# Kernel optimization log

Hardware: AMD Instinct MI355X
Metric: run time of the kernel (lower is better)

The kernel has to match this reference:

```python
import jax, jax.numpy as jnp
import numpy as np

TOPK = 10
NUM_CLASSES = 80
ALPHA = 0.5
BETA = 6.0
EPS = 1e-9


def setup_inputs() -> dict:
    key = jax.random.key(0)
    ks = jax.random.split(key, 7)
    bs, A, n, C = 16, 8400, 64, NUM_CLASSES
    pd_scores = jax.random.uniform(ks[0], (bs, A, C), jnp.float32)
    # valid xyxy boxes inside a 640x640 image
    pxy = jax.random.uniform(ks[1], (bs, A, 2), jnp.float32) * 576.0
    pwh = jax.random.uniform(ks[2], (bs, A, 2), jnp.float32) * 64.0 + 8.0
    pd_bboxes = jnp.concatenate([pxy, pxy + pwh], axis=-1)
    gxy = jax.random.uniform(ks[3], (bs, n, 2), jnp.float32) * 576.0
    gwh = jax.random.uniform(ks[4], (bs, n, 2), jnp.float32) * 64.0 + 8.0
    gt_bboxes = jnp.concatenate([gxy, gxy + gwh], axis=-1)
    anc_points = jax.random.uniform(ks[5], (A, 2), jnp.float32) * 640.0
    gt_labels = jax.random.randint(ks[6], (bs, n, 1), 0, C, dtype=jnp.int32)
    return {"pd_scores": pd_scores, "pd_bboxes": pd_bboxes,
            "anc_points": anc_points, "gt_labels": gt_labels,
            "gt_bboxes": gt_bboxes}


def _iou(gt_bboxes, pd_bboxes, eps=EPS):
    # gt_bboxes: (bs, n, 4), pd_bboxes: (bs, A, 4) -> (bs, n, A)
    b1 = gt_bboxes[:, :, None, :]
    b2 = pd_bboxes[:, None, :, :]
    lt = jnp.maximum(b1[..., :2], b2[..., :2])
    rb = jnp.minimum(b1[..., 2:], b2[..., 2:])
    overlap = jnp.clip(rb - lt, 0).prod(-1)
    area1 = jnp.clip(b1[..., 2:] - b1[..., :2], 0).prod(-1)
    area2 = jnp.clip(b2[..., 2:] - b2[..., :2], 0).prod(-1)
    return overlap / (area1 + area2 - overlap + eps)


def _assign(pd_scores, pd_bboxes, anc_points, gt_labels, gt_bboxes):
    bs, A, C = pd_scores.shape
    n = gt_bboxes.shape[1]
    dt = pd_scores.dtype
    labels = gt_labels[..., 0]                       # (bs, n)
    # ---- box metrics: gather class score per gt (bs, n, A) ----
    bi = jnp.arange(bs)[:, None]                     # (bs, 1)
    bbox_scores = pd_scores[bi, :, labels]           # (bs, n, A)
    overlaps = _iou(gt_bboxes, pd_bboxes)            # (bs, n, A)
    align_metric = bbox_scores ** ALPHA * overlaps ** BETA
    # ---- anchor-center-in-gt mask ----
    lt = gt_bboxes[..., None, :2]                    # (bs, n, 1, 2)
    rb = gt_bboxes[..., None, 2:]
    anc = anc_points[None, None]                     # (1, 1, A, 2)
    deltas_min = jnp.minimum((anc - lt).min(-1), (rb - anc).min(-1))
    mask_in_gts = (deltas_min > EPS).astype(dt)      # (bs, n, A)
    # ---- top-k candidates per gt (scatter-add instead of huge one-hot) ----
    metrics = align_metric * mask_in_gts
    topk_vals, topk_idxs = jax.lax.top_k(metrics, TOPK)
    valid = topk_vals.max(-1, keepdims=True) > EPS
    topk_idxs = jnp.where(valid, topk_idxs, 0)
    bi3 = jnp.arange(bs)[:, None, None]
    ni3 = jnp.arange(n)[None, :, None]
    cnt = jnp.zeros((bs, n, A), dt).at[bi3, ni3, topk_idxs].add(1.0)
    is_in_topk = jnp.where(cnt > 1, jnp.zeros((), dt), cnt)
    mask_pos = is_in_topk * mask_in_gts
    # ---- resolve anchors assigned to multiple gts via highest IoU ----
    fg_mask = mask_pos.sum(-2)                       # (bs, A)
    mask_multi = fg_mask[:, None, :] > 1             # (bs, 1->n, A)
    is_max = jax.nn.one_hot(overlaps.argmax(1), n, axis=1, dtype=dt)  # (bs, n, A)
    mask_pos = jnp.where(mask_multi, is_max, mask_pos)
    fg_mask = mask_pos.sum(-2)
    target_gt_idx = mask_pos.argmax(-2)              # (bs, A)
    # ---- gather targets ----
    flat_idx = target_gt_idx + jnp.arange(bs)[:, None] * n
    target_labels = jnp.maximum(labels.reshape(-1)[flat_idx], 0)
    target_bboxes = gt_bboxes.reshape(-1, 4)[flat_idx]
    target_scores = jax.nn.one_hot(target_labels, C, dtype=dt)
    target_scores = jnp.where(fg_mask[..., None] > 0, target_scores,
                              jnp.zeros((), dt))
    # ---- normalize scores by task-aligned metric ----
    align_metric = align_metric * mask_pos
    pos_align = align_metric.max(-1, keepdims=True)
    pos_over = (overlaps * mask_pos).max(-1, keepdims=True)
    norm = (align_metric * pos_over / (pos_align + EPS)).max(-2)[..., None]
    target_scores = target_scores * norm
    return target_labels, target_bboxes, target_scores, fg_mask > 0


def reference(pd_scores, pd_bboxes, anc_points, gt_labels, gt_bboxes):
    return _assign(pd_scores, pd_bboxes, anc_points, gt_labels, gt_bboxes)
```

## Files before the change

### kernel.cpp

```cpp
#include <hip/hip_runtime.h>

#define TOPK 10
#define EPSF 1e-9f
#define CHUNKS 8

typedef unsigned long long u64;
typedef unsigned int u32;

__global__ __launch_bounds__(256) void k_init(uint4* __restrict__ p, int n16) {
    int i = blockIdx.x * 256 + threadIdx.x;
    if (i < n16) p[i] = make_uint4(0, 0, 0, 0);
}

__global__ __launch_bounds__(256) void k_chunk(
    const float* __restrict__ pd_scores, const float* __restrict__ pd_bboxes,
    const float* __restrict__ anc, const int* __restrict__ gt_labels,
    const float* __restrict__ gt_bboxes,
    float* __restrict__ overlaps, u64* __restrict__ part,
    int A, int n, int C)
{
    const int gw   = blockIdx.x * 4 + (threadIdx.x >> 6);
    const int lane = threadIdx.x & 63;
    const int row  = gw >> 3;
    const int ch   = gw & (CHUNKS - 1);
    const int b    = row / n;
    const int CS   = (A + CHUNKS - 1) / CHUNKS;
    const int a0   = ch * CS;
    const int a1   = min(A, a0 + CS);

    const float4 g = *(const float4*)(gt_bboxes + (size_t)row * 4);
    const int    c = gt_labels[row];
    const float* ps = pd_scores + (size_t)b * A * C + c;
    const float4* pb = (const float4*)(pd_bboxes + (size_t)b * A * 4);
    const float2* an2 = (const float2*)anc;
    const size_t rowbase = (size_t)row * A;
    const float ga = fmaxf(g.z - g.x, 0.f) * fmaxf(g.w - g.y, 0.f);

    u64 tk[TOPK];
    #pragma unroll
    for (int k = 0; k < TOPK; ++k) tk[k] = 0;

    for (int a = a0 + lane; a < a1; a += 64) {
        float4 p = pb[a];
        float ow = fmaxf(fminf(g.z, p.z) - fmaxf(g.x, p.x), 0.f) *
                   fmaxf(fminf(g.w, p.w) - fmaxf(g.y, p.y), 0.f);
        float pa = fmaxf(p.z - p.x, 0.f) * fmaxf(p.w - p.y, 0.f);
        float iou = ow / (ga + pa - ow + EPSF);
        overlaps[rowbase + a] = iou;

        float2 ap = an2[a];
        float dmin = fminf(fminf(ap.x - g.x, ap.y - g.y),
                           fminf(g.z - ap.x, g.w - ap.y));
        float met = 0.f;
        if (dmin > EPSF) met = sqrtf(ps[(size_t)a * C]) * powf(iou, 6.0f);

        u64 key = ((u64)__float_as_uint(met) << 32) | (u32)(0x7fffffff - a);
        if (key > tk[TOPK-1]) {
            tk[TOPK-1] = key;
            #pragma unroll
            for (int k = TOPK-1; k > 0; --k)
                if (tk[k] > tk[k-1]) { u64 t = tk[k]; tk[k] = tk[k-1]; tk[k-1] = t; }
        }
    }

    u64 mine = 0;
    #pragma unroll
    for (int r = 0; r < TOPK; ++r) {
        u64 m = tk[0];
        #pragma unroll
        for (int s = 1; s < 64; s <<= 1) {
            u64 o = __shfl_xor(m, s, 64);
            m = (o > m) ? o : m;
        }
        if (lane == r) mine = m;
        if (tk[0] == m) {
            #pragma unroll
            for (int k = 0; k < TOPK - 1; ++k) tk[k] = tk[k + 1];
            tk[TOPK-1] = 0;
        }
    }
    if (lane < TOPK)
        part[((size_t)row * CHUNKS + ch) * TOPK + lane] = mine;
}

__global__ __launch_bounds__(64) void k_merge(
    const float* __restrict__ anc, const float* __restrict__ gt_bboxes,
    const u64* __restrict__ part, u64* __restrict__ mask64,
    int A, int n, int R)
{
    int row = blockIdx.x * 64 + threadIdx.x;
    if (row >= R) return;
    int b = row / n;
    int j = row - b * n;
    const u64* l = part + (size_t)row * CHUNKS * TOPK;
    const float4 g = *(const float4*)(gt_bboxes + (size_t)row * 4);
    const float2* an2 = (const float2*)anc;

    int p0 = 0, p1 = 0, p2 = 0, p3 = 0, p4 = 0, p5 = 0, p6 = 0, p7 = 0;
    for (int k = 0; k < TOPK; ++k) {
        u64 v0 = (p0 < TOPK) ? l[0*TOPK + p0] : 0;
        u64 v1 = (p1 < TOPK) ? l[1*TOPK + p1] : 0;
        u64 v2 = (p2 < TOPK) ? l[2*TOPK + p2] : 0;
        u64 v3 = (p3 < TOPK) ? l[3*TOPK + p3] : 0;
        u64 v4 = (p4 < TOPK) ? l[4*TOPK + p4] : 0;
        u64 v5 = (p5 < TOPK) ? l[5*TOPK + p5] : 0;
        u64 v6 = (p6 < TOPK) ? l[6*TOPK + p6] : 0;
        u64 v7 = (p7 < TOPK) ? l[7*TOPK + p7] : 0;
        u64 bv = v0; int best = 0;
        if (v1 > bv) { bv = v1; best = 1; }
        if (v2 > bv) { bv = v2; best = 2; }
        if (v3 > bv) { bv = v3; best = 3; }
        if (v4 > bv) { bv = v4; best = 4; }
        if (v5 > bv) { bv = v5; best = 5; }
        if (v6 > bv) { bv = v6; best = 6; }
        if (v7 > bv) { bv = v7; best = 7; }
        p0 += (best == 0); p1 += (best == 1); p2 += (best == 2); p3 += (best == 3);
        p4 += (best == 4); p5 += (best == 5); p6 += (best == 6); p7 += (best == 7);

        if (k == 0) {
            float m0 = __uint_as_float((u32)(bv >> 32));
            if (!(m0 > EPSF)) break;
        }
        int a = 0x7fffffff - (int)(u32)(bv & 0xffffffffu);
        float2 ap = an2[a];
        float dmin = fminf(fminf(ap.x - g.x, ap.y - g.y),
                           fminf(g.z - ap.x, g.w - ap.y));
        if (dmin > EPSF)
            atomicOr(&mask64[(size_t)b * A + a], 1ull << j);
    }
}

__global__ __launch_bounds__(256) void k_col(
    const float* __restrict__ pd_scores,
    const int* __restrict__ gt_labels, const float* __restrict__ gt_bboxes,
    const float* __restrict__ overlaps, u64* __restrict__ mask64,
    float* __restrict__ out_labels, float* __restrict__ out_bboxes,
    float* __restrict__ out_fg,
    float* __restrict__ pos_align, float* __restrict__ pos_over,
    int A, int n, int C)
{
    __shared__ float4 sg[64];
    __shared__ int    sl[64];
    const int b = blockIdx.y;
    const int a = blockIdx.x * 256 + threadIdx.x;
    if (threadIdx.x < n) {
        sg[threadIdx.x] = ((const float4*)gt_bboxes)[b * n + threadIdx.x];
        sl[threadIdx.x] = gt_labels[b * n + threadIdx.x];
    }
    __syncthreads();
    if (a >= A) return;

    const size_t midx = (size_t)b * A + a;
    u64 m = mask64[midx];
    int pc = __popcll(m);
    int jt = 0;
    if (pc > 1) {
        const float* col = overlaps + (size_t)b * n * A + a;
        float bv = col[0]; int bj = 0;
        for (int jj = 1; jj < n; ++jj) {
            float v = col[(size_t)jj * A];
            if (v > bv) { bv = v; bj = jj; }
        }
        jt = bj; mask64[midx] = 1ull << bj; pc = 1;
    } else if (pc == 1) {
        jt = __ffsll(m) - 1;
    }

    int lab = sl[jt];
    out_labels[midx] = (float)(lab < 0 ? 0 : lab);
    ((float4*)out_bboxes)[midx] = sg[jt];
    out_fg[midx] = pc ? 1.f : 0.f;

    if (pc) {
        int rowj = b * n + jt;
        float iou = overlaps[(size_t)rowj * A + a];
        float s = pd_scores[((size_t)b * A + a) * C + lab];
        float al = sqrtf(s) * powf(iou, 6.0f);
        atomicMax((int*)&pos_align[rowj], __float_as_int(al));
        atomicMax((int*)&pos_over[rowj],  __float_as_int(iou));
    }
}

__global__ __launch_bounds__(256) void k_norm(
    const float* __restrict__ pd_scores, const int* __restrict__ gt_labels,
    const float* __restrict__ overlaps, const u64* __restrict__ mask64,
    const float* __restrict__ pos_align, const float* __restrict__ pos_over,
    float* __restrict__ normv, int A, int n, int C, int total)
{
    int idx = blockIdx.x * 256 + threadIdx.x;
    if (idx >= total) return;
    int b = idx / A;
    int a = idx - b * A;
    u64 m = mask64[idx];
    float nm = 0.f;
    if (m) {
        int jj = __ffsll(m) - 1;
        int rowj = b * n + jj;
        float iou = overlaps[(size_t)rowj * A + a];
        float s = pd_scores[(size_t)idx * C + gt_labels[rowj]];
        float al = sqrtf(s) * powf(iou, 6.0f);
        nm = al * pos_over[rowj] / (pos_align[rowj] + EPSF);
    }
    normv[idx] = nm;
}

__global__ __launch_bounds__(256) void k_scores(
    const float* __restrict__ out_labels, const float* __restrict__ out_fg,
    const float* __restrict__ normv, float4* __restrict__ out_scores,
    int C4, int quads)
{
    int idx = blockIdx.x * 256 + threadIdx.x;
    if (idx >= quads) return;
    int ba = idx / C4;
    int q  = idx - ba * C4;
    float4 v = make_float4(0.f, 0.f, 0.f, 0.f);
    if (out_fg[ba] > 0.f) {
        int r = (int)out_labels[ba] - q * 4;
        float nv = normv[ba];
        v.x = (r == 0) ? nv : 0.f;
        v.y = (r == 1) ? nv : 0.f;
        v.z = (r == 2) ? nv : 0.f;
        v.w = (r == 3) ? nv : 0.f;
    }
    out_scores[idx] = v;
}

extern "C" void kernel_launch(void* const* d_in, const int* in_sizes, int n_in,
                              void* d_out, int out_size, void* d_ws, size_t ws_size,
                              hipStream_t stream)
{
    const float* pd_scores = (const float*)d_in[0];
    const float* pd_bboxes = (const float*)d_in[1];
    const float* anc       = (const float*)d_in[2];
    const int*   gt_labels = (const int*)d_in[3];
    const float* gt_bboxes = (const float*)d_in[4];

    const int C  = 80;
    const int A  = in_sizes[2] / 2;
    const int bs = in_sizes[0] / (A * C);
    const int n  = in_sizes[3] / bs;
    const int R  = bs * n;
    const int BA = bs * A;

    size_t off = 0;
    u64*   mask64    = (u64*)((char*)d_ws + off);   off += (size_t)BA * 8;
    float* pos_align = (float*)((char*)d_ws + off); off += (size_t)R * 4;
    float* pos_over  = (float*)((char*)d_ws + off); off += (size_t)R * 4;
    size_t zero_bytes = off;
    float* overlaps  = (float*)((char*)d_ws + off); off += (size_t)R * A * 4;
    float* normv     = (float*)((char*)d_ws + off); off += (size_t)BA * 4;
    u64*   part      = (u64*)((char*)d_ws + off);   off += (size_t)R * CHUNKS * TOPK * 8;

    float* out_labels = (float*)d_out;
    float* out_bboxes = out_labels + (size_t)BA;
    float* out_scores = out_bboxes + (size_t)BA * 4;
    float* out_fg     = out_scores + (size_t)BA * C;

    int n16 = (int)(zero_bytes / 16);
    k_init<<<(n16 + 255) / 256, 256, 0, stream>>>((uint4*)d_ws, n16);

    k_chunk<<<R * CHUNKS / 4, 256, 0, stream>>>(
        pd_scores, pd_bboxes, anc, gt_labels, gt_bboxes, overlaps, part, A, n, C);

    k_merge<<<(R + 63) / 64, 64, 0, stream>>>(
        anc, gt_bboxes, part, mask64, A, n, R);

    k_col<<<dim3((A + 255) / 256, bs), 256, 0, stream>>>(
        pd_scores, gt_labels, gt_bboxes, overlaps, mask64,
        out_labels, out_bboxes, out_fg, pos_align, pos_over, A, n, C);

    k_norm<<<(BA + 255) / 256, 256, 0, stream>>>(
        pd_scores, gt_labels, overlaps, mask64, pos_align, pos_over,
        normv, A, n, C, BA);

    int quads = BA * (C / 4);
    k_scores<<<(quads + 255) / 256, 256, 0, stream>>>(
        out_labels, out_fg, normv, (float4*)out_scores, C / 4, quads);
}
```

Measured before the change: 169.0 us.

## Drop materialized overlaps buffer and recompute IoU on demand

The full (bs, n, A) overlaps array is no longer written. IoU is recomputed from the gt and pred boxes wherever it is needed: in the column argmax, the alignment atomics and the normalization. The chunk kernel now skips IoU and the score gather for anchors outside the gt box and keeps only positive metrics. A wave-parallel merge adds a fallback scan that fills zero-metric top-k slots by index order. This removes roughly 34 MB of writes and strided column reads, in exchange for n IoU evaluations per multi-assigned anchor and a more complex tie-handling path.

```diff
diff --git a/kernel.cpp b/kernel.cpp
--- a/kernel.cpp
+++ b/kernel.cpp
@@ -7,6 +7,27 @@
 typedef unsigned long long u64;
 typedef unsigned int u32;
 
+__device__ __forceinline__ float gt_area(const float4 g) {
+    return fmaxf(g.z - g.x, 0.f) * fmaxf(g.w - g.y, 0.f);
+}
+__device__ __forceinline__ float iou_pair(const float4 g, const float4 p, float ga) {
+    float ow = fmaxf(fminf(g.z, p.z) - fmaxf(g.x, p.x), 0.f) *
+               fmaxf(fminf(g.w, p.w) - fmaxf(g.y, p.y), 0.f);
+    float pa = fmaxf(p.z - p.x, 0.f) * fmaxf(p.w - p.y, 0.f);
+    return ow / (ga + pa - ow + EPSF);
+}
+__device__ __forceinline__ float dmin_f(const float4 g, const float2 ap) {
+    return fminf(fminf(ap.x - g.x, ap.y - g.y), fminf(g.z - ap.x, g.w - ap.y));
+}
+__device__ __forceinline__ u64 wave_max_u64(u64 v) {
+    #pragma unroll
+    for (int s = 1; s < 64; s <<= 1) {
+        u64 o = __shfl_xor(v, s, 64);
+        v = (o > v) ? o : v;
+    }
+    return v;
+}
+
 __global__ __launch_bounds__(256) void k_init(uint4* __restrict__ p, int n16) {
     int i = blockIdx.x * 256 + threadIdx.x;
     if (i < n16) p[i] = make_uint4(0, 0, 0, 0);
@@ -15,8 +36,7 @@
 __global__ __launch_bounds__(256) void k_chunk(
     const float* __restrict__ pd_scores, const float* __restrict__ pd_bboxes,
     const float* __restrict__ anc, const int* __restrict__ gt_labels,
-    const float* __restrict__ gt_bboxes,
-    float* __restrict__ overlaps, u64* __restrict__ part,
+    const float* __restrict__ gt_bboxes, u64* __restrict__ part,
     int A, int n, int C)
 {
     const int gw   = blockIdx.x * 4 + (threadIdx.x >> 6);
@@ -33,45 +53,35 @@
     const float* ps = pd_scores + (size_t)b * A * C + c;
     const float4* pb = (const float4*)(pd_bboxes + (size_t)b * A * 4);
     const float2* an2 = (const float2*)anc;
-    const size_t rowbase = (size_t)row * A;
-    const float ga = fmaxf(g.z - g.x, 0.f) * fmaxf(g.w - g.y, 0.f);
+    const float ga = gt_area(g);
 
     u64 tk[TOPK];
     #pragma unroll
     for (int k = 0; k < TOPK; ++k) tk[k] = 0;
 
     for (int a = a0 + lane; a < a1; a += 64) {
-        float4 p = pb[a];
-        float ow = fmaxf(fminf(g.z, p.z) - fmaxf(g.x, p.x), 0.f) *
-                   fmaxf(fminf(g.w, p.w) - fmaxf(g.y, p.y), 0.f);
-        float pa = fmaxf(p.z - p.x, 0.f) * fmaxf(p.w - p.y, 0.f);
-        float iou = ow / (ga + pa - ow + EPSF);
-        overlaps[rowbase + a] = iou;
-
         float2 ap = an2[a];
-        float dmin = fminf(fminf(ap.x - g.x, ap.y - g.y),
-                           fminf(g.z - ap.x, g.w - ap.y));
-        float met = 0.f;
-        if (dmin > EPSF) met = sqrtf(ps[(size_t)a * C]) * powf(iou, 6.0f);
-
-        u64 key = ((u64)__float_as_uint(met) << 32) | (u32)(0x7fffffff - a);
-        if (key > tk[TOPK-1]) {
-            tk[TOPK-1] = key;
-            #pragma unroll
-            for (int k = TOPK-1; k > 0; --k)
-                if (tk[k] > tk[k-1]) { u64 t = tk[k]; tk[k] = tk[k-1]; tk[k-1] = t; }
+        float dmin = dmin_f(g, ap);
+        if (dmin > EPSF) {
+            float iou = iou_pair(g, pb[a], ga);
+            float met = sqrtf(ps[(size_t)a * C]) * powf(iou, 6.0f);
+            if (met > 0.f) {
+                u64 key = ((u64)__float_as_uint(met) << 32) | (u32)(0x7fffffff - a);
+                if (key > tk[TOPK-1]) {
+                    tk[TOPK-1] = key;
+                    #pragma unroll
+                    for (int k = TOPK-1; k > 0; --k)
+                        if (tk[k] > tk[k-1]) { u64 t = tk[k]; tk[k] = tk[k-1]; tk[k-1] = t; }
+                }
+            }
         }
     }
 
     u64 mine = 0;
     #pragma unroll
     for (int r = 0; r < TOPK; ++r) {
-        u64 m = tk[0];
-        #pragma unroll
-        for (int s = 1; s < 64; s <<= 1) {
-            u64 o = __shfl_xor(m, s, 64);
-            m = (o > m) ? o : m;
-        }
+        u64 m = wave_max_u64(tk[0]);
+        if (m == 0) break;
         if (lane == r) mine = m;
         if (tk[0] == m) {
             #pragma unroll
@@ -83,57 +93,84 @@
         part[((size_t)row * CHUNKS + ch) * TOPK + lane] = mine;
 }
 
-__global__ __launch_bounds__(64) void k_merge(
-    const float* __restrict__ anc, const float* __restrict__ gt_bboxes,
+__global__ __launch_bounds__(256) void k_merge(
+    const float* __restrict__ pd_scores, const float* __restrict__ pd_bboxes,
+    const float* __restrict__ anc, const int* __restrict__ gt_labels,
+    const float* __restrict__ gt_bboxes,
     const u64* __restrict__ part, u64* __restrict__ mask64,
-    int A, int n, int R)
-{
-    int row = blockIdx.x * 64 + threadIdx.x;
-    if (row >= R) return;
-    int b = row / n;
-    int j = row - b * n;
-    const u64* l = part + (size_t)row * CHUNKS * TOPK;
+    int A, int n, int C)
+{
+    const int row  = blockIdx.x * 4 + (threadIdx.x >> 6);
+    const int lane = threadIdx.x & 63;
+    const int b    = row / n;
+    const int j    = row - b * n;
+
+    const u64* l = part + (size_t)row * (CHUNKS * TOPK);
+    u64 e0 = l[lane];
+    u64 e1 = (lane < CHUNKS * TOPK - 64) ? l[64 + lane] : 0;
+
     const float4 g = *(const float4*)(gt_bboxes + (size_t)row * 4);
+    const int    c = gt_labels[row];
+    const float* ps = pd_scores + (size_t)b * A * C + c;
+    const float4* pb = (const float4*)(pd_bboxes + (size_t)b * A * 4);
     const float2* an2 = (const float2*)anc;
-
-    int p0 = 0, p1 = 0, p2 = 0, p3 = 0, p4 = 0, p5 = 0, p6 = 0, p7 = 0;
-    for (int k = 0; k < TOPK; ++k) {
-        u64 v0 = (p0 < TOPK) ? l[0*TOPK + p0] : 0;
-        u64 v1 = (p1 < TOPK) ? l[1*TOPK + p1] : 0;
-        u64 v2 = (p2 < TOPK) ? l[2*TOPK + p2] : 0;
-        u64 v3 = (p3 < TOPK) ? l[3*TOPK + p3] : 0;
-        u64 v4 = (p4 < TOPK) ? l[4*TOPK + p4] : 0;
-        u64 v5 = (p5 < TOPK) ? l[5*TOPK + p5] : 0;
-        u64 v6 = (p6 < TOPK) ? l[6*TOPK + p6] : 0;
-        u64 v7 = (p7 < TOPK) ? l[7*TOPK + p7] : 0;
-        u64 bv = v0; int best = 0;
-        if (v1 > bv) { bv = v1; best = 1; }
-        if (v2 > bv) { bv = v2; best = 2; }
-        if (v3 > bv) { bv = v3; best = 3; }
-        if (v4 > bv) { bv = v4; best = 4; }
-        if (v5 > bv) { bv = v5; best = 5; }
-        if (v6 > bv) { bv = v6; best = 6; }
-        if (v7 > bv) { bv = v7; best = 7; }
-        p0 += (best == 0); p1 += (best == 1); p2 += (best == 2); p3 += (best == 3);
-        p4 += (best == 4); p5 += (best == 5); p6 += (best == 6); p7 += (best == 7);
-
-        if (k == 0) {
-            float m0 = __uint_as_float((u32)(bv >> 32));
-            if (!(m0 > EPSF)) break;
-        }
-        int a = 0x7fffffff - (int)(u32)(bv & 0xffffffffu);
-        float2 ap = an2[a];
-        float dmin = fminf(fminf(ap.x - g.x, ap.y - g.y),
-                           fminf(g.z - ap.x, g.w - ap.y));
-        if (dmin > EPSF)
-            atomicOr(&mask64[(size_t)b * A + a], 1ull << j);
+    const float ga = gt_area(g);
+    u64* mrow = mask64 + (size_t)b * A;
+
+    int npos = 0;
+    bool invalid = false;
+    u64 mine = 0;
+    for (int r = 0; r < TOPK; ++r) {
+        u64 me = (e0 > e1) ? e0 : e1;
+        u64 m = wave_max_u64(me);
+        if (r == 0) {
+            float m0 = __uint_as_float((u32)(m >> 32));
+            if (!(m0 > EPSF)) { invalid = true; break; }
+        }
+        if (m == 0) break;
+        if (lane == r) mine = m;
+        if (e0 == m) e0 = 0; else if (e1 == m) e1 = 0;
+        ++npos;
+    }
+
+    if (lane < npos) {
+        int a = 0x7fffffff - (int)(u32)(mine & 0xffffffffu);
+        if (dmin_f(g, an2[a]) > EPSF)
+            atomicOr(&mrow[a], 1ull << j);
+    }
+
+    if (!invalid) {
+        int need = TOPK - npos;
+        int base = 0;
+        while (need > 0 && base < A) {
+            int a = base + lane;
+            float met = 1.f;
+            float dmin = -1.f;
+            if (a < A) {
+                float2 ap = an2[a];
+                dmin = dmin_f(g, ap);
+                met = 0.f;
+                if (dmin > EPSF) {
+                    float iou = iou_pair(g, pb[a], ga);
+                    met = sqrtf(ps[(size_t)a * C]) * powf(iou, 6.0f);
+                }
+            }
+            u64 zm = __ballot(met == 0.f);
+            int cnt = __popcll(zm);
+            int take = (need < cnt) ? need : cnt;
+            int rank = __popcll(zm & ((1ull << lane) - 1ull));
+            if (met == 0.f && rank < take && dmin > EPSF)
+                atomicOr(&mrow[a], 1ull << j);
+            need -= take;
+            base += 64;
+        }
     }
 }
 
 __global__ __launch_bounds__(256) void k_col(
-    const float* __restrict__ pd_scores,
+    const float* __restrict__ pd_scores, const float* __restrict__ pd_bboxes,
     const int* __restrict__ gt_labels, const float* __restrict__ gt_bboxes,
-    const float* __restrict__ overlaps, u64* __restrict__ mask64,
+    u64* __restrict__ mask64,
     float* __restrict__ out_labels, float* __restrict__ out_bboxes,
     float* __restrict__ out_fg,
     float* __restrict__ pos_align, float* __restrict__ pos_over,
@@ -154,11 +191,13 @@
     u64 m = mask64[midx];
     int pc = __popcll(m);
     int jt = 0;
+    float4 p;
+    if (pc) p = ((const float4*)pd_bboxes)[midx];
     if (pc > 1) {
-        const float* col = overlaps + (size_t)b * n * A + a;
-        float bv = col[0]; int bj = 0;
+        float bv = iou_pair(sg[0], p, gt_area(sg[0]));
+        int bj = 0;
         for (int jj = 1; jj < n; ++jj) {
-            float v = col[(size_t)jj * A];
+            float v = iou_pair(sg[jj], p, gt_area(sg[jj]));
             if (v > bv) { bv = v; bj = jj; }
         }
         jt = bj; mask64[midx] = 1ull << bj; pc = 1;
@@ -173,8 +212,9 @@
 
     if (pc) {
         int rowj = b * n + jt;
-        float iou = overlaps[(size_t)rowj * A + a];
-        float s = pd_scores[((size_t)b * A + a) * C + lab];
+        float4 gj = sg[jt];
+        float iou = iou_pair(gj, p, gt_area(gj));
+        float s = pd_scores[midx * C + lab];
         float al = sqrtf(s) * powf(iou, 6.0f);
         atomicMax((int*)&pos_align[rowj], __float_as_int(al));
         atomicMax((int*)&pos_over[rowj],  __float_as_int(iou));
@@ -182,21 +222,23 @@
 }
 
 __global__ __launch_bounds__(256) void k_norm(
-    const float* __restrict__ pd_scores, const int* __restrict__ gt_labels,
-    const float* __restrict__ overlaps, const u64* __restrict__ mask64,
+    const float* __restrict__ pd_scores, const float* __restrict__ pd_bboxes,
+    const int* __restrict__ gt_labels, const float* __restrict__ gt_bboxes,
+    const u64* __restrict__ mask64,
     const float* __restrict__ pos_align, const float* __restrict__ pos_over,
     float* __restrict__ normv, int A, int n, int C, int total)
 {
     int idx = blockIdx.x * 256 + threadIdx.x;
     if (idx >= total) return;
     int b = idx / A;
-    int a = idx - b * A;
     u64 m = mask64[idx];
     float nm = 0.f;
     if (m) {
-        int jj = __ffsll(m) - 1;
-        int rowj = b * n + jj;
-        float iou = overlaps[(size_t)rowj * A + a];
+        int jt = __ffsll(m) - 1;
+        int rowj = b * n + jt;
+        float4 gj = *(const float4*)(gt_bboxes + (size_t)rowj * 4);
+        float4 p  = ((const float4*)pd_bboxes)[idx];
+        float iou = iou_pair(gj, p, gt_area(gj));
         float s = pd_scores[(size_t)idx * C + gt_labels[rowj]];
         float al = sqrtf(s) * powf(iou, 6.0f);
         nm = al * pos_over[rowj] / (pos_align[rowj] + EPSF);
@@ -247,9 +289,8 @@
     float* pos_align = (float*)((char*)d_ws + off); off += (size_t)R * 4;
     float* pos_over  = (float*)((char*)d_ws + off); off += (size_t)R * 4;
     size_t zero_bytes = off;
-    float* overlaps  = (float*)((char*)d_ws + off); off += (size_t)R * A * 4;
-    float* normv     = (float*)((char*)d_ws + off); off += (size_t)BA * 4;
-    u64*   part      = (u64*)((char*)d_ws + off);   off += (size_t)R * CHUNKS * TOPK * 8;
+    float* normv = (float*)((char*)d_ws + off);     off += (size_t)BA * 4;
+    u64*   part  = (u64*)((char*)d_ws + off);       off += (size_t)R * CHUNKS * TOPK * 8;
 
     float* out_labels = (float*)d_out;
     float* out_bboxes = out_labels + (size_t)BA;
@@ -260,18 +301,18 @@
     k_init<<<(n16 + 255) / 256, 256, 0, stream>>>((uint4*)d_ws, n16);
 
     k_chunk<<<R * CHUNKS / 4, 256, 0, stream>>>(
-        pd_scores, pd_bboxes, anc, gt_labels, gt_bboxes, overlaps, part, A, n, C);
-
-    k_merge<<<(R + 63) / 64, 64, 0, stream>>>(
-        anc, gt_bboxes, part, mask64, A, n, R);
+        pd_scores, pd_bboxes, anc, gt_labels, gt_bboxes, part, A, n, C);
+
+    k_merge<<<R / 4, 256, 0, stream>>>(
+        pd_scores, pd_bboxes, anc, gt_labels, gt_bboxes, part, mask64, A, n, C);
 
     k_col<<<dim3((A + 255) / 256, bs), 256, 0, stream>>>(
-        pd_scores, gt_labels, gt_bboxes, overlaps, mask64,
+        pd_scores, pd_bboxes, gt_labels, gt_bboxes, mask64,
         out_labels, out_bboxes, out_fg, pos_align, pos_over, A, n, C);
 
     k_norm<<<(BA + 255) / 256, 256, 0, stream>>>(
-        pd_scores, gt_labels, overlaps, mask64, pos_align, pos_over,
-        normv, A, n, C, BA);
+        pd_scores, pd_bboxes, gt_labels, gt_bboxes, mask64,
+        pos_align, pos_over, normv, A, n, C, BA);
 
     int quads = BA * (C / 4);
     k_scores<<<(quads + 255) / 256, 256, 0, stream>>>(
```

Measured after the change: 151.1 us. 1.12x faster.
